# Performance work log

Measured on AMD Instinct MI355X. Metric: run time of the kernel, lower is better.

## Reference

```python
import jax, jax.numpy as jnp
import numpy as np

B, IN_DIM, HID, DIM, M = 4096, 256, 200, 512, 256


def setup_inputs() -> dict:
    key = jax.random.key(0)
    ks = jax.random.split(key, 9)
    x = jax.random.normal(ks[0], (B, IN_DIM), dtype=jnp.float32)
    # per-sample polytope RHS; strictly positive so y=0 is always feasible
    b = jax.random.uniform(ks[1], (B, M), dtype=jnp.float32) + 1.0
    W1 = jax.random.normal(ks[2], (IN_DIM, HID), dtype=jnp.float32) / np.sqrt(IN_DIM)
    b1 = jnp.zeros((HID,), dtype=jnp.float32)
    W2 = jax.random.normal(ks[3], (HID, HID), dtype=jnp.float32) / np.sqrt(HID)
    b2 = jnp.zeros((HID,), dtype=jnp.float32)
    W3 = jax.random.normal(ks[4], (HID, DIM), dtype=jnp.float32) / np.sqrt(HID)
    b3 = jnp.zeros((DIM,), dtype=jnp.float32)
    # constraint matrix A: polytope {y : A y <= b}
    A = jax.random.normal(ks[5], (M, DIM), dtype=jnp.float32) / np.sqrt(DIM)
    return {"x": x, "b": b, "W1": W1, "b1": b1, "W2": W2, "b2": b2,
            "W3": W3, "b3": b3, "A": A, "step": 0, "n_iter": 100}


def _mlp(x, W1, b1, W2, b2, W3, b3):
    h = jax.nn.relu(x @ W1 + b1)
    h = jax.nn.relu(h @ W2 + b2)
    return h @ W3 + b3  # [B, DIM]


def _project(y0, b, A, n_iter):
    """Euclidean projection of y0 onto {y : A y <= b} via dual projected gradient.
    y(lam) = y0 - A^T lam;  lam <- relu(lam + t (A y(lam) - b))."""
    t = 1.0 / jnp.sum(A * A)  # 1/||A||_F^2 <= 1/sigma_max(A)^2 -> convergent step

    def body(lam, _):
        y = y0 - lam @ A                      # [B, DIM]
        lam = jax.nn.relu(lam + t * (y @ A.T - b))  # [B, M]
        return lam, None

    lam0 = jnp.zeros_like(b)
    lam, _ = jax.lax.scan(body, lam0, None, length=n_iter)
    return y0 - lam @ A


def reference(x, b, W1, b1, W2, b2, W3, b3, A, step, n_iter):
    y0 = _mlp(x, W1, b1, W2, b2, W3, b3)
    # optax.linear_schedule(0.0, 0.0, 2000, 300) is identically zero
    alpha = jnp.float32(0.0)
    y = _project(y0, b, A, n_iter)
    return (1.0 - alpha) * y + alpha * y0
```

## Files before the change

### kernel.cpp

```cpp
#include <hip/hip_runtime.h>
#include <hip/hip_bf16.h>
#include <stdint.h>


typedef __attribute__((ext_vector_type(8))) short bf16x8;
typedef __attribute__((ext_vector_type(4))) float f32x4;
typedef __attribute__((ext_vector_type(4))) unsigned short u16x4;

__device__ __forceinline__ unsigned short f2b(float f) {
  union { float f; uint32_t u; } v; v.f = f;
  uint32_t r = (v.u + 0x7FFFu + ((v.u >> 16) & 1u)) >> 16;
  return (unsigned short)r;
}
__device__ __forceinline__ float b2f(unsigned short h) {
  union { uint32_t u; float f; } v; v.u = ((uint32_t)h) << 16;
  return v.f;
}
__device__ __forceinline__ unsigned int pk2(float a, float b) {
  __hip_bfloat162 h = __float22bfloat162_rn(make_float2(a, b));
  unsigned int u; __builtin_memcpy(&u, &h, 4); return u;
}
__device__ __forceinline__ float ldf(const void* p, int idx, int f32f) {
  return f32f ? ((const float*)p)[idx] : b2f(((const unsigned short*)p)[idx]);
}
__device__ __forceinline__ f32x4 mfma16(bf16x8 a, bf16x8 b, f32x4 c) {
  return __builtin_amdgcn_mfma_f32_16x16x32_bf16(a, b, c, 0, 0, 0);
}
__device__ __forceinline__ bf16x8 ld8(const void* p, int idx, int f32f) {
  bf16x8 r;
  if (f32f) {
    float4 a0 = *(const float4*)((const float*)p + idx);
    float4 a1 = *(const float4*)((const float*)p + idx + 4);
    r[0]=(short)f2b(a0.x); r[1]=(short)f2b(a0.y); r[2]=(short)f2b(a0.z); r[3]=(short)f2b(a0.w);
    r[4]=(short)f2b(a1.x); r[5]=(short)f2b(a1.y); r[6]=(short)f2b(a1.z); r[7]=(short)f2b(a1.w);
  } else {
    r = *(const bf16x8*)((const unsigned short*)p + idx);
  }
  return r;
}
__device__ __forceinline__ int sniff(const void* p) {
  unsigned short h = ((const unsigned short*)p)[threadIdx.x & 63];
  unsigned e = (h >> 7) & 0xFFu;
  return (__ballot(e >= 132u) != 0ull) ? 1 : 0;
}

__device__ __forceinline__ void swiz_one(const void* __restrict__ src,
                                         unsigned short* __restrict__ dst, int e,
                                         int Ksrc, int Nsrc, int ld, bool trans,
                                         int NCT, int f32f) {
  const int j = e & 7, lane = (e >> 3) & 63, rest = e >> 9;
  const int nt = rest % NCT, kk = rest / NCT;
  const int k = kk * 32 + ((lane >> 4) << 3) + j;
  const int n = nt * 16 + (lane & 15);
  unsigned short v = 0;
  if (k < Ksrc && n < Nsrc)
    v = f2b(ldf(src, trans ? n * ld + k : k * ld + n, f32f));
  dst[e] = v;
}

__global__ __launch_bounds__(256) void prep_kernel(
    const void* __restrict__ W1, const void* __restrict__ W2,
    const void* __restrict__ W3, const void* __restrict__ Am,
    unsigned short* __restrict__ Gsw, float* __restrict__ slot,
    unsigned short* __restrict__ W1sw, unsigned short* __restrict__ W2sw,
    unsigned short* __restrict__ W3sw, unsigned short* __restrict__ ATsw,
    unsigned short* __restrict__ Asw) {
  const int f32f = sniff(Am);
  const int tid = threadIdx.x;
  if (blockIdx.x < 256) {
    if (tid >= 64) return;
    const int lane = tid, r16 = lane & 15, q = lane >> 4;
    const int ti = blockIdx.x >> 4, tj = blockIdx.x & 15;
    const int rowA = (16 * ti + r16) * 512;
    const int rowB = (16 * tj + r16) * 512;
    f32x4 acc = {0.f, 0.f, 0.f, 0.f};
    #pragma unroll
    for (int kk = 0; kk < 16; ++kk) {
      const int col = 32 * kk + 8 * q;
      bf16x8 afr = ld8(Am, rowA + col, f32f);
      bf16x8 bfr = ld8(Am, rowB + col, f32f);
      acc = mfma16(afr, bfr, acc);
    }
    #pragma unroll
    for (int rg = 0; rg < 4; ++rg) {
      const int mrow = 16 * ti + 4 * q + rg;
      const int kk2 = mrow >> 5, q2 = (mrow >> 3) & 3, j = mrow & 7;
      Gsw[((kk2 * 16 + tj) * 64 + (q2 * 16 + r16)) * 8 + j] = f2b(acc[rg]);
    }
    if (ti == tj) {
      float d = ((r16 >> 2) == q) ? acc[r16 & 3] : 0.0f;
      #pragma unroll
      for (int off = 32; off >= 1; off >>= 1) d += __shfl_xor(d, off, 64);
      if (lane == 0) slot[ti] = d;
    }
    return;
  }
  int idx = (blockIdx.x - 256) * 256 + tid;
  if (idx < 53248)  { swiz_one(W1, W1sw, idx, 256, 200, 200, false, 13, f32f); return; }
  idx -= 53248;
  if (idx < 46592)  { swiz_one(W2, W2sw, idx, 200, 200, 200, false, 13, f32f); return; }
  idx -= 46592;
  if (idx < 114688) { swiz_one(W3, W3sw, idx, 200, 512, 512, false, 32, f32f); return; }
  idx -= 114688;
  if (idx < 131072) { swiz_one(Am, ATsw, idx, 512, 256, 512, true, 16, f32f); return; }
  idx -= 131072;
  swiz_one(Am, Asw, idx, 256, 512, 512, false, 32, f32f);
}

__global__ __launch_bounds__(512, 2) void mega_kernel(
    const void* __restrict__ x,
    const void* __restrict__ bmat,
    const void* __restrict__ b1,
    const void* __restrict__ b2,
    const void* __restrict__ b3,
    const float* __restrict__ slot,
    const unsigned short* __restrict__ Gsw,
    const unsigned short* __restrict__ W1sw,
    const unsigned short* __restrict__ W2sw,
    const unsigned short* __restrict__ W3sw,
    const unsigned short* __restrict__ ATsw,
    const unsigned short* __restrict__ Asw,
    float* __restrict__ out)
{
  __shared__ __attribute__((aligned(16))) unsigned short xbuf[16 * 264];
  __shared__ __attribute__((aligned(16))) unsigned short hbuf[16 * 232];
  __shared__ __attribute__((aligned(16))) unsigned short ybuf[16 * 520];
  __shared__ __attribute__((aligned(16))) unsigned short lbuf[2][16 * 264];
  __shared__ __attribute__((aligned(16))) float yf32[16 * 516];

  const int tid = threadIdx.x;
  const int lane = tid & 63;
  const int w = tid >> 6;
  const int r16 = lane & 15;
  const int q = lane >> 4;
  const int rowbase = blockIdx.x << 4;
  const int f32f = sniff(x);

  {
    const int rr = tid >> 5;
    const int c8 = (tid & 31) << 3;
    if (f32f) {
      const float4* sp = (const float4*)((const float*)x + (rowbase + rr) * 256 + c8);
      float4 v0 = sp[0], v1 = sp[1];
      u16x4 p0 = {f2b(v0.x), f2b(v0.y), f2b(v0.z), f2b(v0.w)};
      u16x4 p1 = {f2b(v1.x), f2b(v1.y), f2b(v1.z), f2b(v1.w)};
      *(u16x4*)&xbuf[rr * 264 + c8]     = p0;
      *(u16x4*)&xbuf[rr * 264 + c8 + 4] = p1;
    } else {
      *(bf16x8*)&xbuf[rr * 264 + c8] =
          *(const bf16x8*)((const unsigned short*)x + (rowbase + rr) * 256 + c8);
    }
    if (tid < 256) hbuf[(tid >> 4) * 232 + 208 + (tid & 15)] = 0;
  }
  __syncthreads();
  float tr = 0.0f;
  #pragma unroll
  for (int i = 0; i < 16; ++i) tr += slot[i];
  const float t = 1.0f / tr;

  f32x4 a1[2];
  #pragma unroll
  for (int i = 0; i < 2; ++i) a1[i] = (f32x4){0.f, 0.f, 0.f, 0.f};
  #pragma unroll
  for (int kk = 0; kk < 8; ++kk) {
    bf16x8 bx = *(const bf16x8*)&xbuf[r16 * 264 + 32 * kk + 8 * q];
    #pragma unroll
    for (int i = 0; i < 2; ++i) {
      const int nt = w + 8 * i;
      if (nt < 13) {
        bf16x8 af = *(const bf16x8*)(W1sw + ((kk * 13 + nt) * 64 + lane) * 8);
        a1[i] = mfma16(af, bx, a1[i]);
      }
    }
  }
  #pragma unroll
  for (int i = 0; i < 2; ++i) {
    const int nt = w + 8 * i;
    if (nt < 13) {
      u16x4 pk;
      #pragma unroll
      for (int rg = 0; rg < 4; ++rg) {
        const int n = 16 * nt + 4 * q + rg;
        const float bias = (n < 200) ? ldf(b1, n, f32f) : 0.0f;
        pk[rg] = f2b(fmaxf(a1[i][rg] + bias, 0.0f));
      }
      *(u16x4*)&hbuf[r16 * 232 + 16 * nt + 4 * q] = pk;
    }
  }
  __syncthreads();

  f32x4 a2[2];
  #pragma unroll
  for (int i = 0; i < 2; ++i) a2[i] = (f32x4){0.f, 0.f, 0.f, 0.f};
  #pragma unroll
  for (int kk = 0; kk < 7; ++kk) {
    bf16x8 bh = *(const bf16x8*)&hbuf[r16 * 232 + 32 * kk + 8 * q];
    #pragma unroll
    for (int i = 0; i < 2; ++i) {
      const int nt = w + 8 * i;
      if (nt < 13) {
        bf16x8 af = *(const bf16x8*)(W2sw + ((kk * 13 + nt) * 64 + lane) * 8);
        a2[i] = mfma16(af, bh, a2[i]);
      }
    }
  }
  __syncthreads();
  #pragma unroll
  for (int i = 0; i < 2; ++i) {
    const int nt = w + 8 * i;
    if (nt < 13) {
      u16x4 pk;
      #pragma unroll
      for (int rg = 0; rg < 4; ++rg) {
        const int n = 16 * nt + 4 * q + rg;
        const float bias = (n < 200) ? ldf(b2, n, f32f) : 0.0f;
        pk[rg] = f2b(fmaxf(a2[i][rg] + bias, 0.0f));
      }
      *(u16x4*)&hbuf[r16 * 232 + 16 * nt + 4 * q] = pk;
    }
  }
  __syncthreads();

  {
    f32x4 y0a[4];
    #pragma unroll
    for (int i = 0; i < 4; ++i) y0a[i] = (f32x4){0.f, 0.f, 0.f, 0.f};
    #pragma unroll
    for (int kk = 0; kk < 7; ++kk) {
      bf16x8 bh = *(const bf16x8*)&hbuf[r16 * 232 + 32 * kk + 8 * q];
      #pragma unroll
      for (int i = 0; i < 4; ++i) {
        const int nt = 4 * w + i;
        bf16x8 af = *(const bf16x8*)(W3sw + ((kk * 32 + nt) * 64 + lane) * 8);
        y0a[i] = mfma16(af, bh, y0a[i]);
      }
    }
    #pragma unroll
    for (int i = 0; i < 4; ++i) {
      const int nt = 4 * w + i;
      u16x4 pk;
      #pragma unroll
      for (int rg = 0; rg < 4; ++rg) {
        y0a[i][rg] += ldf(b3, 16 * nt + 4 * q + rg, f32f);
        pk[rg] = f2b(y0a[i][rg]);
      }
      *(u16x4*)&ybuf[r16 * 520 + 16 * nt + 4 * q] = pk;
      float4 sf = {y0a[i][0], y0a[i][1], y0a[i][2], y0a[i][3]};
      *(float4*)&yf32[r16 * 516 + 16 * nt + 4 * q] = sf;
    }
  }
  __syncthreads();

  f32x4 tc[2], base[2];
  {
    f32x4 cacc[2];
    #pragma unroll
    for (int i = 0; i < 2; ++i) {
      const int mt = w + 8 * i;
      if (f32f) {
        float4 bb = *(const float4*)((const float*)bmat + (rowbase + r16) * 256 + 16 * mt + 4 * q);
        cacc[i] = (f32x4){-bb.x, -bb.y, -bb.z, -bb.w};
      } else {
        u16x4 bb = *(const u16x4*)((const unsigned short*)bmat + (rowbase + r16) * 256 + 16 * mt + 4 * q);
        #pragma unroll
        for (int rg = 0; rg < 4; ++rg) cacc[i][rg] = -b2f(bb[rg]);
      }
    }
    #pragma unroll
    for (int kk = 0; kk < 16; ++kk) {
      bf16x8 by = *(const bf16x8*)&ybuf[r16 * 520 + 32 * kk + 8 * q];
      #pragma unroll
      for (int i = 0; i < 2; ++i) {
        bf16x8 af = *(const bf16x8*)(ATsw + ((kk * 16 + w + 8 * i) * 64 + lane) * 8);
        cacc[i] = mfma16(af, by, cacc[i]);
      }
    }
    #pragma unroll
    for (int i = 0; i < 2; ++i) {
      #pragma unroll
      for (int rg = 0; rg < 4; ++rg) {
        tc[i][rg] = t * cacc[i][rg];
        base[i][rg] = fmaxf(tc[i][rg], 0.0f) + tc[i][rg];
      }
      const unsigned int lo = pk2(fmaxf(tc[i][0], 0.f), fmaxf(tc[i][1], 0.f));
      const unsigned int hi = pk2(fmaxf(tc[i][2], 0.f), fmaxf(tc[i][3], 0.f));
      *(uint2*)&lbuf[0][r16 * 264 + 16 * (w + 8 * i) + 4 * q] = make_uint2(lo, hi);
    }
  }

  #define GLD(j, i) (*(const bf16x8*)(Gsw + (((j) * 16 + w + 8 * (i)) * 64 + lane) * 8))
  bf16x8 gA0 = GLD(0,0), gA1 = GLD(1,0), gA2 = GLD(2,0), gA3 = GLD(3,0);
  bf16x8 gA4 = GLD(4,0), gA5 = GLD(5,0), gA6 = GLD(6,0), gA7 = GLD(7,0);
  bf16x8 gB0 = GLD(0,1), gB1 = GLD(1,1), gB2 = GLD(2,1), gB3 = GLD(3,1);
  bf16x8 gB4 = GLD(4,1), gB5 = GLD(5,1), gB6 = GLD(6,1), gB7 = GLD(7,1);
  #undef GLD
  asm volatile("" : "+v"(gA0), "+v"(gA1), "+v"(gA2), "+v"(gA3),
                    "+v"(gA4), "+v"(gA5), "+v"(gA6), "+v"(gA7),
                    "+v"(gB0), "+v"(gB1), "+v"(gB2), "+v"(gB3),
                    "+v"(gB4), "+v"(gB5), "+v"(gB6), "+v"(gB7));
  __syncthreads();

  int cur = 0;
  for (int it = 0; it < 98; ++it) {
    const unsigned short* lb = &lbuf[cur][r16 * 264 + 8 * q];
    bf16x8 bl[8];
    #pragma unroll
    for (int j = 0; j < 8; ++j)
      bl[j] = *(const bf16x8*)(lb + 32 * j);
    f32x4 acc0 = {0.f, 0.f, 0.f, 0.f}, acc1 = {0.f, 0.f, 0.f, 0.f};
    acc0 = mfma16(gA0, bl[0], acc0);  acc1 = mfma16(gB0, bl[0], acc1);
    acc0 = mfma16(gA1, bl[1], acc0);  acc1 = mfma16(gB1, bl[1], acc1);
    acc0 = mfma16(gA2, bl[2], acc0);  acc1 = mfma16(gB2, bl[2], acc1);
    acc0 = mfma16(gA3, bl[3], acc0);  acc1 = mfma16(gB3, bl[3], acc1);
    acc0 = mfma16(gA4, bl[4], acc0);  acc1 = mfma16(gB4, bl[4], acc1);
    acc0 = mfma16(gA5, bl[5], acc0);  acc1 = mfma16(gB5, bl[5], acc1);
    acc0 = mfma16(gA6, bl[6], acc0);  acc1 = mfma16(gB6, bl[6], acc1);
    acc0 = mfma16(gA7, bl[7], acc0);  acc1 = mfma16(gB7, bl[7], acc1);
    const int nxt = cur ^ 1;
    {
      f32x4 v;
      #pragma unroll
      for (int rg = 0; rg < 4; ++rg)
        v[rg] = fmaxf(fmaf(-t, acc0[rg], base[0][rg]), 0.0f);
      *(uint2*)&lbuf[nxt][r16 * 264 + 16 * w + 4 * q] =
          make_uint2(pk2(v[0], v[1]), pk2(v[2], v[3]));
      #pragma unroll
      for (int rg = 0; rg < 4; ++rg) base[0][rg] = v[rg] + tc[0][rg];
    }
    {
      f32x4 v;
      #pragma unroll
      for (int rg = 0; rg < 4; ++rg)
        v[rg] = fmaxf(fmaf(-t, acc1[rg], base[1][rg]), 0.0f);
      *(uint2*)&lbuf[nxt][r16 * 264 + 16 * (w + 8) + 4 * q] =
          make_uint2(pk2(v[0], v[1]), pk2(v[2], v[3]));
      #pragma unroll
      for (int rg = 0; rg < 4; ++rg) base[1][rg] = v[rg] + tc[1][rg];
    }
    __syncthreads();
    cur = nxt;
  }

  {
    const unsigned short* lb = &lbuf[cur][r16 * 264 + 8 * q];
    bf16x8 bl[8];
    #pragma unroll
    for (int j = 0; j < 8; ++j)
      bl[j] = *(const bf16x8*)(lb + 32 * j);
    f32x4 acc0 = {0.f, 0.f, 0.f, 0.f}, acc1 = {0.f, 0.f, 0.f, 0.f};
    acc0 = mfma16(gA0, bl[0], acc0);  acc1 = mfma16(gB0, bl[0], acc1);
    acc0 = mfma16(gA1, bl[1], acc0);  acc1 = mfma16(gB1, bl[1], acc1);
    acc0 = mfma16(gA2, bl[2], acc0);  acc1 = mfma16(gB2, bl[2], acc1);
    acc0 = mfma16(gA3, bl[3], acc0);  acc1 = mfma16(gB3, bl[3], acc1);
    acc0 = mfma16(gA4, bl[4], acc0);  acc1 = mfma16(gB4, bl[4], acc1);
    acc0 = mfma16(gA5, bl[5], acc0);  acc1 = mfma16(gB5, bl[5], acc1);
    acc0 = mfma16(gA6, bl[6], acc0);  acc1 = mfma16(gB6, bl[6], acc1);
    acc0 = mfma16(gA7, bl[7], acc0);  acc1 = mfma16(gB7, bl[7], acc1);
    const int nxt = cur ^ 1;
    {
      f32x4 v;
      #pragma unroll
      for (int rg = 0; rg < 4; ++rg)
        v[rg] = fmaxf(fmaf(-t, acc0[rg], base[0][rg]), 0.0f);
      *(uint2*)&lbuf[nxt][r16 * 264 + 16 * w + 4 * q] =
          make_uint2(pk2(v[0], v[1]) ^ 0x80008000u, pk2(v[2], v[3]) ^ 0x80008000u);
    }
    {
      f32x4 v;
      #pragma unroll
      for (int rg = 0; rg < 4; ++rg)
        v[rg] = fmaxf(fmaf(-t, acc1[rg], base[1][rg]), 0.0f);
      *(uint2*)&lbuf[nxt][r16 * 264 + 16 * (w + 8) + 4 * q] =
          make_uint2(pk2(v[0], v[1]) ^ 0x80008000u, pk2(v[2], v[3]) ^ 0x80008000u);
    }
    __syncthreads();
    cur = nxt;
  }

  f32x4 yo[4];
  #pragma unroll
  for (int i = 0; i < 4; ++i) {
    float4 v = *(const float4*)&yf32[r16 * 516 + 16 * (4 * w + i) + 4 * q];
    yo[i] = (f32x4){v.x, v.y, v.z, v.w};
  }
  #pragma unroll
  for (int kk = 0; kk < 8; ++kk) {
    bf16x8 bl = *(const bf16x8*)&lbuf[cur][r16 * 264 + 32 * kk + 8 * q];
    #pragma unroll
    for (int i = 0; i < 4; ++i) {
      bf16x8 af = *(const bf16x8*)(Asw + ((kk * 32 + 4 * w + i) * 64 + lane) * 8);
      yo[i] = mfma16(af, bl, yo[i]);
    }
  }
  #pragma unroll
  for (int i = 0; i < 4; ++i) {
    const int nt = 4 * w + i;
    float4 st = {yo[i][0], yo[i][1], yo[i][2], yo[i][3]};
    *(float4*)(out + (size_t)(rowbase + r16) * 512 + 16 * nt + 4 * q) = st;
  }
}

extern "C" void kernel_launch(void* const* d_in, const int* in_sizes, int n_in,
                              void* d_out, int out_size, void* d_ws, size_t ws_size,
                              hipStream_t stream) {
  const void* x  = d_in[0];
  const void* bm = d_in[1];
  const void* W1 = d_in[2];
  const void* b1 = d_in[3];
  const void* W2 = d_in[4];
  const void* b2 = d_in[5];
  const void* W3 = d_in[6];
  const void* b3 = d_in[7];
  const void* Am = d_in[8];

  float* slot = (float*)d_ws;
  unsigned short* Gsw  = (unsigned short*)d_ws + 128;
  unsigned short* W1sw = Gsw  + 65536;
  unsigned short* W2sw = W1sw + 53248;
  unsigned short* W3sw = W2sw + 46592;
  unsigned short* ATsw = W3sw + 114688;
  unsigned short* Asw  = ATsw + 131072;

  prep_kernel<<<2118, 256, 0, stream>>>(W1, W2, W3, Am, Gsw, slot,
                                        W1sw, W2sw, W3sw, ATsw, Asw);
  mega_kernel<<<256, 512, 0, stream>>>(x, bm, b1, b2, b3, slot,
                                       Gsw, W1sw, W2sw, W3sw, ATsw, Asw,
                                       (float*)d_out);
}
```

Measured before the change: 81.11 us.

## Run dual iteration loop on four waves with four M-tiles each

```diff
diff --git a/kernel.cpp b/kernel.cpp
--- a/kernel.cpp
+++ b/kernel.cpp
@@ -251,12 +251,12 @@
   }
   __syncthreads();
 
-  f32x4 tc[2], base[2];
-  {
-    f32x4 cacc[2];
-    #pragma unroll
-    for (int i = 0; i < 2; ++i) {
-      const int mt = w + 8 * i;
+  f32x4 tc[4], base[4];
+  if (w < 4) {
+    f32x4 cacc[4];
+    #pragma unroll
+    for (int i = 0; i < 4; ++i) {
+      const int mt = w + 4 * i;
       if (f32f) {
         float4 bb = *(const float4*)((const float*)bmat + (rowbase + r16) * 256 + 16 * mt + 4 * q);
         cacc[i] = (f32x4){-bb.x, -bb.y, -bb.z, -bb.w};
@@ -270,13 +270,13 @@
     for (int kk = 0; kk < 16; ++kk) {
       bf16x8 by = *(const bf16x8*)&ybuf[r16 * 520 + 32 * kk + 8 * q];
       #pragma unroll
-      for (int i = 0; i < 2; ++i) {
-        bf16x8 af = *(const bf16x8*)(ATsw + ((kk * 16 + w + 8 * i) * 64 + lane) * 8);
+      for (int i = 0; i < 4; ++i) {
+        bf16x8 af = *(const bf16x8*)(ATsw + ((kk * 16 + w + 4 * i) * 64 + lane) * 8);
         cacc[i] = mfma16(af, by, cacc[i]);
       }
     }
     #pragma unroll
-    for (int i = 0; i < 2; ++i) {
+    for (int i = 0; i < 4; ++i) {
       #pragma unroll
       for (int rg = 0; rg < 4; ++rg) {
         tc[i][rg] = t * cacc[i][rg];
@@ -284,98 +284,102 @@
       }
       const unsigned int lo = pk2(fmaxf(tc[i][0], 0.f), fmaxf(tc[i][1], 0.f));
       const unsigned int hi = pk2(fmaxf(tc[i][2], 0.f), fmaxf(tc[i][3], 0.f));
-      *(uint2*)&lbuf[0][r16 * 264 + 16 * (w + 8 * i) + 4 * q] = make_uint2(lo, hi);
-    }
-  }
-
-  #define GLD(j, i) (*(const bf16x8*)(Gsw + (((j) * 16 + w + 8 * (i)) * 64 + lane) * 8))
-  bf16x8 gA0 = GLD(0,0), gA1 = GLD(1,0), gA2 = GLD(2,0), gA3 = GLD(3,0);
-  bf16x8 gA4 = GLD(4,0), gA5 = GLD(5,0), gA6 = GLD(6,0), gA7 = GLD(7,0);
-  bf16x8 gB0 = GLD(0,1), gB1 = GLD(1,1), gB2 = GLD(2,1), gB3 = GLD(3,1);
-  bf16x8 gB4 = GLD(4,1), gB5 = GLD(5,1), gB6 = GLD(6,1), gB7 = GLD(7,1);
-  #undef GLD
-  asm volatile("" : "+v"(gA0), "+v"(gA1), "+v"(gA2), "+v"(gA3),
-                    "+v"(gA4), "+v"(gA5), "+v"(gA6), "+v"(gA7),
-                    "+v"(gB0), "+v"(gB1), "+v"(gB2), "+v"(gB3),
-                    "+v"(gB4), "+v"(gB5), "+v"(gB6), "+v"(gB7));
-  __syncthreads();
-
+      *(uint2*)&lbuf[0][r16 * 264 + 16 * (w + 4 * i) + 4 * q] = make_uint2(lo, hi);
+    }
+  }
+
+  bf16x8 gA0, gA1, gA2, gA3, gA4, gA5, gA6, gA7;
+  bf16x8 gB0, gB1, gB2, gB3, gB4, gB5, gB6, gB7;
+  bf16x8 gC0, gC1, gC2, gC3, gC4, gC5, gC6, gC7;
+  bf16x8 gD0, gD1, gD2, gD3, gD4, gD5, gD6, gD7;
+  if (w < 4) {
+    #define GLD(j, i) (*(const bf16x8*)(Gsw + (((j) * 16 + w + 4 * (i)) * 64 + lane) * 8))
+    gA0 = GLD(0,0); gA1 = GLD(1,0); gA2 = GLD(2,0); gA3 = GLD(3,0);
+    gA4 = GLD(4,0); gA5 = GLD(5,0); gA6 = GLD(6,0); gA7 = GLD(7,0);
+    gB0 = GLD(0,1); gB1 = GLD(1,1); gB2 = GLD(2,1); gB3 = GLD(3,1);
+    gB4 = GLD(4,1); gB5 = GLD(5,1); gB6 = GLD(6,1); gB7 = GLD(7,1);
+    gC0 = GLD(0,2); gC1 = GLD(1,2); gC2 = GLD(2,2); gC3 = GLD(3,2);
+    gC4 = GLD(4,2); gC5 = GLD(5,2); gC6 = GLD(6,2); gC7 = GLD(7,2);
+    gD0 = GLD(0,3); gD1 = GLD(1,3); gD2 = GLD(2,3); gD3 = GLD(3,3);
+    gD4 = GLD(4,3); gD5 = GLD(5,3); gD6 = GLD(6,3); gD7 = GLD(7,3);
+    #undef GLD
+    asm volatile("" : "+v"(gA0), "+v"(gA1), "+v"(gA2), "+v"(gA3),
+                      "+v"(gA4), "+v"(gA5), "+v"(gA6), "+v"(gA7),
+                      "+v"(gB0), "+v"(gB1), "+v"(gB2), "+v"(gB3),
+                      "+v"(gB4), "+v"(gB5), "+v"(gB6), "+v"(gB7));
+    asm volatile("" : "+v"(gC0), "+v"(gC1), "+v"(gC2), "+v"(gC3),
+                      "+v"(gC4), "+v"(gC5), "+v"(gC6), "+v"(gC7),
+                      "+v"(gD0), "+v"(gD1), "+v"(gD2), "+v"(gD3),
+                      "+v"(gD4), "+v"(gD5), "+v"(gD6), "+v"(gD7));
+  }
+  __syncthreads();
+
+  #define PGD_J(j, blv) \
+    acc0 = mfma16(gA##j, blv, acc0); acc1 = mfma16(gB##j, blv, acc1); \
+    acc2 = mfma16(gC##j, blv, acc2); acc3 = mfma16(gD##j, blv, acc3);
   int cur = 0;
-  for (int it = 0; it < 98; ++it) {
-    const unsigned short* lb = &lbuf[cur][r16 * 264 + 8 * q];
-    bf16x8 bl[8];
-    #pragma unroll
-    for (int j = 0; j < 8; ++j)
-      bl[j] = *(const bf16x8*)(lb + 32 * j);
-    f32x4 acc0 = {0.f, 0.f, 0.f, 0.f}, acc1 = {0.f, 0.f, 0.f, 0.f};
-    acc0 = mfma16(gA0, bl[0], acc0);  acc1 = mfma16(gB0, bl[0], acc1);
-    acc0 = mfma16(gA1, bl[1], acc0);  acc1 = mfma16(gB1, bl[1], acc1);
-    acc0 = mfma16(gA2, bl[2], acc0);  acc1 = mfma16(gB2, bl[2], acc1);
-    acc0 = mfma16(gA3, bl[3], acc0);  acc1 = mfma16(gB3, bl[3], acc1);
-    acc0 = mfma16(gA4, bl[4], acc0);  acc1 = mfma16(gB4, bl[4], acc1);
-    acc0 = mfma16(gA5, bl[5], acc0);  acc1 = mfma16(gB5, bl[5], acc1);
-    acc0 = mfma16(gA6, bl[6], acc0);  acc1 = mfma16(gB6, bl[6], acc1);
-    acc0 = mfma16(gA7, bl[7], acc0);  acc1 = mfma16(gB7, bl[7], acc1);
-    const int nxt = cur ^ 1;
-    {
-      f32x4 v;
-      #pragma unroll
-      for (int rg = 0; rg < 4; ++rg)
-        v[rg] = fmaxf(fmaf(-t, acc0[rg], base[0][rg]), 0.0f);
-      *(uint2*)&lbuf[nxt][r16 * 264 + 16 * w + 4 * q] =
-          make_uint2(pk2(v[0], v[1]), pk2(v[2], v[3]));
-      #pragma unroll
-      for (int rg = 0; rg < 4; ++rg) base[0][rg] = v[rg] + tc[0][rg];
-    }
-    {
-      f32x4 v;
-      #pragma unroll
-      for (int rg = 0; rg < 4; ++rg)
-        v[rg] = fmaxf(fmaf(-t, acc1[rg], base[1][rg]), 0.0f);
-      *(uint2*)&lbuf[nxt][r16 * 264 + 16 * (w + 8) + 4 * q] =
-          make_uint2(pk2(v[0], v[1]), pk2(v[2], v[3]));
-      #pragma unroll
-      for (int rg = 0; rg < 4; ++rg) base[1][rg] = v[rg] + tc[1][rg];
+  for (int it = 0; it < 99; ++it) {
+    if (w < 4) {
+      const unsigned short* lb = &lbuf[cur][r16 * 264 + 8 * q];
+      const bf16x8 bl0 = *(const bf16x8*)(lb);
+      const bf16x8 bl1 = *(const bf16x8*)(lb + 32);
+      const bf16x8 bl2 = *(const bf16x8*)(lb + 64);
+      const bf16x8 bl3 = *(const bf16x8*)(lb + 96);
+      const bf16x8 bl4 = *(const bf16x8*)(lb + 128);
+      const bf16x8 bl5 = *(const bf16x8*)(lb + 160);
+      const bf16x8 bl6 = *(const bf16x8*)(lb + 192);
+      const bf16x8 bl7 = *(const bf16x8*)(lb + 224);
+      f32x4 acc0 = {0.f, 0.f, 0.f, 0.f}, acc1 = {0.f, 0.f, 0.f, 0.f};
+      f32x4 acc2 = {0.f, 0.f, 0.f, 0.f}, acc3 = {0.f, 0.f, 0.f, 0.f};
+      PGD_J(0, bl0)  PGD_J(1, bl1)  PGD_J(2, bl2)  PGD_J(3, bl3)
+      PGD_J(4, bl4)  PGD_J(5, bl5)  PGD_J(6, bl6)  PGD_J(7, bl7)
+      const unsigned int sx = (it == 98) ? 0x80008000u : 0u;
+      const int nxt = cur ^ 1;
+      {
+        f32x4 v;
+        #pragma unroll
+        for (int rg = 0; rg < 4; ++rg)
+          v[rg] = fmaxf(fmaf(-t, acc0[rg], base[0][rg]), 0.0f);
+        *(uint2*)&lbuf[nxt][r16 * 264 + 16 * w + 4 * q] =
+            make_uint2(pk2(v[0], v[1]) ^ sx, pk2(v[2], v[3]) ^ sx);
+        #pragma unroll
+        for (int rg = 0; rg < 4; ++rg) base[0][rg] = v[rg] + tc[0][rg];
+      }
+      {
+        f32x4 v;
+        #pragma unroll
+        for (int rg = 0; rg < 4; ++rg)
+          v[rg] = fmaxf(fmaf(-t, acc1[rg], base[1][rg]), 0.0f);
+        *(uint2*)&lbuf[nxt][r16 * 264 + 16 * (w + 4) + 4 * q] =
+            make_uint2(pk2(v[0], v[1]) ^ sx, pk2(v[2], v[3]) ^ sx);
+        #pragma unroll
+        for (int rg = 0; rg < 4; ++rg) base[1][rg] = v[rg] + tc[1][rg];
+      }
+      {
+        f32x4 v;
+        #pragma unroll
+        for (int rg = 0; rg < 4; ++rg)
+          v[rg] = fmaxf(fmaf(-t, acc2[rg], base[2][rg]), 0.0f);
+        *(uint2*)&lbuf[nxt][r16 * 264 + 16 * (w + 8) + 4 * q] =
+            make_uint2(pk2(v[0], v[1]) ^ sx, pk2(v[2], v[3]) ^ sx);
+        #pragma unroll
+        for (int rg = 0; rg < 4; ++rg) base[2][rg] = v[rg] + tc[2][rg];
+      }
+      {
+        f32x4 v;
+        #pragma unroll
+        for (int rg = 0; rg < 4; ++rg)
+          v[rg] = fmaxf(fmaf(-t, acc3[rg], base[3][rg]), 0.0f);
+        *(uint2*)&lbuf[nxt][r16 * 264 + 16 * (w + 12) + 4 * q] =
+            make_uint2(pk2(v[0], v[1]) ^ sx, pk2(v[2], v[3]) ^ sx);
+        #pragma unroll
+        for (int rg = 0; rg < 4; ++rg) base[3][rg] = v[rg] + tc[3][rg];
+      }
     }
     __syncthreads();
-    cur = nxt;
-  }
-
-  {
-    const unsigned short* lb = &lbuf[cur][r16 * 264 + 8 * q];
-    bf16x8 bl[8];
-    #pragma unroll
-    for (int j = 0; j < 8; ++j)
-      bl[j] = *(const bf16x8*)(lb + 32 * j);
-    f32x4 acc0 = {0.f, 0.f, 0.f, 0.f}, acc1 = {0.f, 0.f, 0.f, 0.f};
-    acc0 = mfma16(gA0, bl[0], acc0);  acc1 = mfma16(gB0, bl[0], acc1);
-    acc0 = mfma16(gA1, bl[1], acc0);  acc1 = mfma16(gB1, bl[1], acc1);
-    acc0 = mfma16(gA2, bl[2], acc0);  acc1 = mfma16(gB2, bl[2], acc1);
-    acc0 = mfma16(gA3, bl[3], acc0);  acc1 = mfma16(gB3, bl[3], acc1);
-    acc0 = mfma16(gA4, bl[4], acc0);  acc1 = mfma16(gB4, bl[4], acc1);
-    acc0 = mfma16(gA5, bl[5], acc0);  acc1 = mfma16(gB5, bl[5], acc1);
-    acc0 = mfma16(gA6, bl[6], acc0);  acc1 = mfma16(gB6, bl[6], acc1);
-    acc0 = mfma16(gA7, bl[7], acc0);  acc1 = mfma16(gB7, bl[7], acc1);
-    const int nxt = cur ^ 1;
-    {
-      f32x4 v;
-      #pragma unroll
-      for (int rg = 0; rg < 4; ++rg)
-        v[rg] = fmaxf(fmaf(-t, acc0[rg], base[0][rg]), 0.0f);
-      *(uint2*)&lbuf[nxt][r16 * 264 + 16 * w + 4 * q] =
-          make_uint2(pk2(v[0], v[1]) ^ 0x80008000u, pk2(v[2], v[3]) ^ 0x80008000u);
-    }
-    {
-      f32x4 v;
-      #pragma unroll
-      for (int rg = 0; rg < 4; ++rg)
-        v[rg] = fmaxf(fmaf(-t, acc1[rg], base[1][rg]), 0.0f);
-      *(uint2*)&lbuf[nxt][r16 * 264 + 16 * (w + 8) + 4 * q] =
-          make_uint2(pk2(v[0], v[1]) ^ 0x80008000u, pk2(v[2], v[3]) ^ 0x80008000u);
-    }
-    __syncthreads();
-    cur = nxt;
-  }
+    cur ^= 1;
+  }
+  #undef PGD_J
 
   f32x4 yo[4];
   #pragma unroll
```

Result: slower. 89.30 us (+10.1%).

## Replace per-iteration block barrier with per-wave release/acquire flags in dual loop

Applied to the files above, without the earlier changes.

```diff
diff --git a/kernel.cpp b/kernel.cpp
--- a/kernel.cpp
+++ b/kernel.cpp
@@ -127,6 +127,7 @@
   __shared__ __attribute__((aligned(16))) unsigned short ybuf[16 * 520];
   __shared__ __attribute__((aligned(16))) unsigned short lbuf[2][16 * 264];
   __shared__ __attribute__((aligned(16))) float yf32[16 * 516];
+  __shared__ unsigned flags[8];
 
   const int tid = threadIdx.x;
   const int lane = tid & 63;
@@ -151,6 +152,7 @@
           *(const bf16x8*)((const unsigned short*)x + (rowbase + rr) * 256 + c8);
     }
     if (tid < 256) hbuf[(tid >> 4) * 232 + 208 + (tid & 15)] = 0;
+    if (tid < 8) flags[tid] = 0;
   }
   __syncthreads();
   float tr = 0.0f;
@@ -251,12 +253,13 @@
   }
   __syncthreads();
 
+  const int t0 = 2 * w, t1 = 2 * w + 1;
   f32x4 tc[2], base[2];
   {
     f32x4 cacc[2];
     #pragma unroll
     for (int i = 0; i < 2; ++i) {
-      const int mt = w + 8 * i;
+      const int mt = t0 + i;
       if (f32f) {
         float4 bb = *(const float4*)((const float*)bmat + (rowbase + r16) * 256 + 16 * mt + 4 * q);
         cacc[i] = (f32x4){-bb.x, -bb.y, -bb.z, -bb.w};
@@ -271,7 +274,7 @@
       bf16x8 by = *(const bf16x8*)&ybuf[r16 * 520 + 32 * kk + 8 * q];
       #pragma unroll
       for (int i = 0; i < 2; ++i) {
-        bf16x8 af = *(const bf16x8*)(ATsw + ((kk * 16 + w + 8 * i) * 64 + lane) * 8);
+        bf16x8 af = *(const bf16x8*)(ATsw + ((kk * 16 + t0 + i) * 64 + lane) * 8);
         cacc[i] = mfma16(af, by, cacc[i]);
       }
     }
@@ -284,46 +287,47 @@
       }
       const unsigned int lo = pk2(fmaxf(tc[i][0], 0.f), fmaxf(tc[i][1], 0.f));
       const unsigned int hi = pk2(fmaxf(tc[i][2], 0.f), fmaxf(tc[i][3], 0.f));
-      *(uint2*)&lbuf[0][r16 * 264 + 16 * (w + 8 * i) + 4 * q] = make_uint2(lo, hi);
-    }
-  }
-
-  #define GLD(j, i) (*(const bf16x8*)(Gsw + (((j) * 16 + w + 8 * (i)) * 64 + lane) * 8))
-  bf16x8 gA0 = GLD(0,0), gA1 = GLD(1,0), gA2 = GLD(2,0), gA3 = GLD(3,0);
-  bf16x8 gA4 = GLD(4,0), gA5 = GLD(5,0), gA6 = GLD(6,0), gA7 = GLD(7,0);
-  bf16x8 gB0 = GLD(0,1), gB1 = GLD(1,1), gB2 = GLD(2,1), gB3 = GLD(3,1);
-  bf16x8 gB4 = GLD(4,1), gB5 = GLD(5,1), gB6 = GLD(6,1), gB7 = GLD(7,1);
-  #undef GLD
-  asm volatile("" : "+v"(gA0), "+v"(gA1), "+v"(gA2), "+v"(gA3),
-                    "+v"(gA4), "+v"(gA5), "+v"(gA6), "+v"(gA7),
-                    "+v"(gB0), "+v"(gB1), "+v"(gB2), "+v"(gB3),
-                    "+v"(gB4), "+v"(gB5), "+v"(gB6), "+v"(gB7));
-  __syncthreads();
-
+      *(uint2*)&lbuf[0][r16 * 264 + 16 * (t0 + i) + 4 * q] = make_uint2(lo, hi);
+    }
+  }
+
+  #define GFR(cs, mt) (*(const bf16x8*)(Gsw + (((cs) * 16 + (mt)) * 64 + lane) * 8))
+  bf16x8 g0a = GFR((w + 0) & 7, t0), g0b = GFR((w + 0) & 7, t1);
+  bf16x8 g1a = GFR((w + 1) & 7, t0), g1b = GFR((w + 1) & 7, t1);
+  bf16x8 g2a = GFR((w + 2) & 7, t0), g2b = GFR((w + 2) & 7, t1);
+  bf16x8 g3a = GFR((w + 3) & 7, t0), g3b = GFR((w + 3) & 7, t1);
+  bf16x8 g4a = GFR((w + 4) & 7, t0), g4b = GFR((w + 4) & 7, t1);
+  bf16x8 g5a = GFR((w + 5) & 7, t0), g5b = GFR((w + 5) & 7, t1);
+  bf16x8 g6a = GFR((w + 6) & 7, t0), g6b = GFR((w + 6) & 7, t1);
+  bf16x8 g7a = GFR((w + 7) & 7, t0), g7b = GFR((w + 7) & 7, t1);
+  #undef GFR
+  asm volatile("" : "+v"(g0a), "+v"(g1a), "+v"(g2a), "+v"(g3a),
+                    "+v"(g4a), "+v"(g5a), "+v"(g6a), "+v"(g7a),
+                    "+v"(g0b), "+v"(g1b), "+v"(g2b), "+v"(g3b),
+                    "+v"(g4b), "+v"(g5b), "+v"(g6b), "+v"(g7b));
+  __syncthreads();
+
+  #define STEP(s, ga, gb) {                                                    \
+    const int cs = (w + (s)) & 7;                                              \
+    while (__hip_atomic_load(&flags[cs], __ATOMIC_ACQUIRE,                     \
+                             __HIP_MEMORY_SCOPE_WORKGROUP) < (unsigned)it) {}  \
+    const bf16x8 bl = *(const bf16x8*)&lbuf[cur][r16 * 264 + 32 * cs + 8 * q]; \
+    acc0 = mfma16(ga, bl, acc0);                                               \
+    acc1 = mfma16(gb, bl, acc1); }
   int cur = 0;
-  for (int it = 0; it < 98; ++it) {
-    const unsigned short* lb = &lbuf[cur][r16 * 264 + 8 * q];
-    bf16x8 bl[8];
-    #pragma unroll
-    for (int j = 0; j < 8; ++j)
-      bl[j] = *(const bf16x8*)(lb + 32 * j);
+  for (int it = 0; it < 99; ++it) {
     f32x4 acc0 = {0.f, 0.f, 0.f, 0.f}, acc1 = {0.f, 0.f, 0.f, 0.f};
-    acc0 = mfma16(gA0, bl[0], acc0);  acc1 = mfma16(gB0, bl[0], acc1);
-    acc0 = mfma16(gA1, bl[1], acc0);  acc1 = mfma16(gB1, bl[1], acc1);
-    acc0 = mfma16(gA2, bl[2], acc0);  acc1 = mfma16(gB2, bl[2], acc1);
-    acc0 = mfma16(gA3, bl[3], acc0);  acc1 = mfma16(gB3, bl[3], acc1);
-    acc0 = mfma16(gA4, bl[4], acc0);  acc1 = mfma16(gB4, bl[4], acc1);
-    acc0 = mfma16(gA5, bl[5], acc0);  acc1 = mfma16(gB5, bl[5], acc1);
-    acc0 = mfma16(gA6, bl[6], acc0);  acc1 = mfma16(gB6, bl[6], acc1);
-    acc0 = mfma16(gA7, bl[7], acc0);  acc1 = mfma16(gB7, bl[7], acc1);
+    STEP(0, g0a, g0b)  STEP(1, g1a, g1b)  STEP(2, g2a, g2b)  STEP(3, g3a, g3b)
+    STEP(4, g4a, g4b)  STEP(5, g5a, g5b)  STEP(6, g6a, g6b)  STEP(7, g7a, g7b)
+    const unsigned int sx = (it == 98) ? 0x80008000u : 0u;
     const int nxt = cur ^ 1;
     {
       f32x4 v;
       #pragma unroll
       for (int rg = 0; rg < 4; ++rg)
         v[rg] = fmaxf(fmaf(-t, acc0[rg], base[0][rg]), 0.0f);
-      *(uint2*)&lbuf[nxt][r16 * 264 + 16 * w + 4 * q] =
-          make_uint2(pk2(v[0], v[1]), pk2(v[2], v[3]));
+      *(uint2*)&lbuf[nxt][r16 * 264 + 16 * t0 + 4 * q] =
+          make_uint2(pk2(v[0], v[1]) ^ sx, pk2(v[2], v[3]) ^ sx);
       #pragma unroll
       for (int rg = 0; rg < 4; ++rg) base[0][rg] = v[rg] + tc[0][rg];
     }
@@ -332,50 +336,18 @@
       #pragma unroll
       for (int rg = 0; rg < 4; ++rg)
         v[rg] = fmaxf(fmaf(-t, acc1[rg], base[1][rg]), 0.0f);
-      *(uint2*)&lbuf[nxt][r16 * 264 + 16 * (w + 8) + 4 * q] =
-          make_uint2(pk2(v[0], v[1]), pk2(v[2], v[3]));
+      *(uint2*)&lbuf[nxt][r16 * 264 + 16 * t1 + 4 * q] =
+          make_uint2(pk2(v[0], v[1]) ^ sx, pk2(v[2], v[3]) ^ sx);
       #pragma unroll
       for (int rg = 0; rg < 4; ++rg) base[1][rg] = v[rg] + tc[1][rg];
     }
-    __syncthreads();
+    if (lane == 0)
+      __hip_atomic_store(&flags[w], (unsigned)(it + 1), __ATOMIC_RELEASE,
+                         __HIP_MEMORY_SCOPE_WORKGROUP);
     cur = nxt;
   }
-
-  {
-    const unsigned short* lb = &lbuf[cur][r16 * 264 + 8 * q];
-    bf16x8 bl[8];
-    #pragma unroll
-    for (int j = 0; j < 8; ++j)
-      bl[j] = *(const bf16x8*)(lb + 32 * j);
-    f32x4 acc0 = {0.f, 0.f, 0.f, 0.f}, acc1 = {0.f, 0.f, 0.f, 0.f};
-    acc0 = mfma16(gA0, bl[0], acc0);  acc1 = mfma16(gB0, bl[0], acc1);
-    acc0 = mfma16(gA1, bl[1], acc0);  acc1 = mfma16(gB1, bl[1], acc1);
-    acc0 = mfma16(gA2, bl[2], acc0);  acc1 = mfma16(gB2, bl[2], acc1);
-    acc0 = mfma16(gA3, bl[3], acc0);  acc1 = mfma16(gB3, bl[3], acc1);
-    acc0 = mfma16(gA4, bl[4], acc0);  acc1 = mfma16(gB4, bl[4], acc1);
-    acc0 = mfma16(gA5, bl[5], acc0);  acc1 = mfma16(gB5, bl[5], acc1);
-    acc0 = mfma16(gA6, bl[6], acc0);  acc1 = mfma16(gB6, bl[6], acc1);
-    acc0 = mfma16(gA7, bl[7], acc0);  acc1 = mfma16(gB7, bl[7], acc1);
-    const int nxt = cur ^ 1;
-    {
-      f32x4 v;
-      #pragma unroll
-      for (int rg = 0; rg < 4; ++rg)
-        v[rg] = fmaxf(fmaf(-t, acc0[rg], base[0][rg]), 0.0f);
-      *(uint2*)&lbuf[nxt][r16 * 264 + 16 * w + 4 * q] =
-          make_uint2(pk2(v[0], v[1]) ^ 0x80008000u, pk2(v[2], v[3]) ^ 0x80008000u);
-    }
-    {
-      f32x4 v;
-      #pragma unroll
-      for (int rg = 0; rg < 4; ++rg)
-        v[rg] = fmaxf(fmaf(-t, acc1[rg], base[1][rg]), 0.0f);
-      *(uint2*)&lbuf[nxt][r16 * 264 + 16 * (w + 8) + 4 * q] =
-          make_uint2(pk2(v[0], v[1]) ^ 0x80008000u, pk2(v[2], v[3]) ^ 0x80008000u);
-    }
-    __syncthreads();
-    cur = nxt;
-  }
+  #undef STEP
+  __syncthreads();
 
   f32x4 yo[4];
   #pragma unroll
```

New measurement: 118.8 us. 46.5% more time.
